# Kernel optimization log

Measured on AMD Instinct MI355X. Metric: run time of the kernel, lower is better.

Reference implementation:

```python
import jax, jax.numpy as jnp
import numpy as np

N_LAYER, N_HEAD, D_MODEL, D_K, D_HIDDEN = 8, 8, 512, 64, 2048
N_CONTEXT, N_DICT, MAG = 1024, 8192, 0.05
B, T = 8, 1024


def _sinusoidal_pos(n_context, d_model):
    i2 = np.arange(0, d_model, 2)
    inv = 1.0 / (10000.0 ** (i2 / d_model))
    ang = np.arange(n_context, dtype=np.float32)[:, None] * inv[None, :]
    pe = np.zeros((1, n_context, d_model), np.float32)
    pe[0, :, 0::2] = np.sin(ang)
    pe[0, :, 1::2] = np.cos(ang)
    return jnp.asarray(pe)


def setup_inputs() -> dict:
    key = jax.random.key(0)
    ks = jax.random.split(key, 10)
    p = lambda k, *s: jax.random.normal(k, s, jnp.float32) * MAG
    return {
        "x": jax.random.randint(ks[0], (B, T), 0, N_DICT),
        "last_only": False,
        "capture_stats": False,
        "embedding": p(ks[1], N_DICT, D_MODEL),
        "pos_embedding": _sinusoidal_pos(N_CONTEXT, D_MODEL),  # fixedpos='True', not trained
        "wq": p(ks[2], N_LAYER, N_HEAD, D_MODEL, D_K),
        "wk": p(ks[3], N_LAYER, N_HEAD, D_MODEL, D_K),
        "wv": p(ks[4], N_LAYER, N_HEAD, D_MODEL, D_MODEL),
        "mlp0": p(ks[5], N_LAYER, D_MODEL, D_HIDDEN),
        "mlpb": p(ks[6], N_LAYER, 1, D_HIDDEN),
        "mlp1": p(ks[7], N_LAYER, D_HIDDEN, D_MODEL),
        "unembedding": p(ks[8], D_MODEL, N_DICT),
        "bias": p(ks[9], 1, 1, N_DICT),
    }


def _ln(x):
    # torch LayerNorm(elementwise_affine=False, bias=False), eps=1e-5, biased var
    mu = jnp.mean(x, axis=-1, keepdims=True)
    var = jnp.mean((x - mu) ** 2, axis=-1, keepdims=True)
    return (x - mu) * jax.lax.rsqrt(var + 1e-5)


def reference(x, last_only, capture_stats, embedding, pos_embedding,
              wq, wk, wv, mlp0, mlpb, mlp1, unembedding, bias):
    del capture_stats  # stats path disabled (capture_stats=False)
    t = x.shape[1]
    h = embedding[x] + pos_embedding[:, :t, :]   # [B,T,M]
    h = _ln(h)                                    # enorm='True', lmul = 1/ldiv = 1
    mask = jnp.tril(jnp.ones((t, t), dtype=bool))

    def layer(h, params):
        wq_l, wk_l, wv_l, m0, mb, m1 = params
        q = jnp.einsum('btm,hmq->bhtq', h, wq_l)
        k = jnp.einsum('bom,hmk->bhok', h, wk_l)
        v = jnp.einsum('bom,hmv->bhov', h, wv_l)
        attn = jnp.einsum('bhtq,bhoq->bhto', q, k)
        # exp(clamp(.,max=50)) then tril then sum-normalize (NOT softmax)
        attn = jnp.where(mask, jnp.exp(jnp.minimum(attn, 50.0)), 0.0)
        attn = attn / (jnp.sum(attn, axis=-1, keepdims=True) + 1e-10)
        vsum = jnp.einsum('bhto,bhov->btv', attn, v)  # sums over heads
        h = _ln(h + vsum)                              # amul = 1, lmul = 1
        y = jax.nn.relu(jnp.einsum('btm,mh->bth', h, m0) + mb)
        y = jnp.einsum('bth,hm->btm', y, m1)
        h = _ln(h + y)                                 # pmul = 1, lmul = 1
        return h, None

    h, _ = jax.lax.scan(layer, h, (wq, wk, wv, mlp0, mlpb, mlp1))
    if last_only:
        h = h[:, -1:, :]
    return jnp.einsum('btm,md->btd', h, unembedding) + bias
```

## Files before the change

kernel.cpp:

```cpp
#include <hip/hip_runtime.h>
#include <hip/hip_bf16.h>

#define BB 8
#define TT 1024
#define DM 512
#define NH 8
#define DK 64
#define DH 2048
#define NL 8
#define ND 8192

typedef __attribute__((ext_vector_type(8))) short short8v;
typedef __attribute__((ext_vector_type(8))) _Float16 f16x8;
typedef __attribute__((ext_vector_type(4))) float f32x4;
typedef __attribute__((ext_vector_type(4))) unsigned short ushort4v;
typedef unsigned short u16;

#define MFMA16(a, b, c) __builtin_amdgcn_mfma_f32_16x16x32_bf16(a, b, c, 0, 0, 0)
#define MFMAH(a, b, c)  __builtin_amdgcn_mfma_f32_16x16x32_f16(a, b, c, 0, 0, 0)

__device__ __forceinline__ u16 bf16_bits(float f) {
  union { __hip_bfloat16 h; u16 u; } cv;
  cv.h = __float2bfloat16(f);
  return cv.u;
}
__device__ __forceinline__ float bits_to_f32(u16 u) {
  union { __hip_bfloat16 h; u16 u; } cv;
  cv.u = u;
  return __bfloat162float(cv.h);
}

__device__ __forceinline__ void gload16(const void* g, void* l) {
  __builtin_amdgcn_global_load_lds(
      (const __attribute__((address_space(1))) unsigned int*)g,
      (__attribute__((address_space(3))) unsigned int*)l, 16, 0, 0);
}

#define WAITVM(N) asm volatile("s_waitcnt vmcnt(" #N ")" ::: "memory")
#define WAITLGKM() asm volatile("s_waitcnt lgkmcnt(0)" ::: "memory")
#define BAR() { __builtin_amdgcn_s_barrier(); asm volatile("" ::: "memory"); }

#define WL_SZ 4718592
#define WR0  41943040
#define WR1 100663296

__device__ __forceinline__ void block_reduce2(float& a, float& b) {
  #pragma unroll
  for (int off = 32; off > 0; off >>= 1) {
    a += __shfl_down(a, off, 64);
    b += __shfl_down(b, off, 64);
  }
  __shared__ float sa[4], sb[4];
  int w = threadIdx.x >> 6;
  if ((threadIdx.x & 63) == 0) { sa[w] = a; sb[w] = b; }
  __syncthreads();
  if (threadIdx.x == 0) {
    sa[0] = sa[0] + sa[1] + sa[2] + sa[3];
    sb[0] = sb[0] + sb[1] + sb[2] + sb[3];
  }
  __syncthreads();
  a = sa[0]; b = sb[0];
}

__global__ __launch_bounds__(256) void embed_ln_kernel(
    const int* __restrict__ x, const float* __restrict__ emb,
    const float* __restrict__ pos, float* __restrict__ h,
    u16* __restrict__ hh, _Float16* __restrict__ hf) {
  int bt = blockIdx.x;
  int t = bt & (TT - 1);
  int tid = threadIdx.x;
  int row = x[bt];
  float v0 = emb[(size_t)row * DM + tid]       + pos[(size_t)t * DM + tid];
  float v1 = emb[(size_t)row * DM + tid + 256] + pos[(size_t)t * DM + tid + 256];
  float s = v0 + v1, sq = v0 * v0 + v1 * v1;
  block_reduce2(s, sq);
  float mu  = s * (1.0f / DM);
  float var = sq * (1.0f / DM) - mu * mu;
  float rs  = rsqrtf(var + 1e-5f);
  float r0 = (v0 - mu) * rs, r1 = (v1 - mu) * rs;
  h[(size_t)bt * DM + tid] = r0;
  h[(size_t)bt * DM + tid + 256] = r1;
  hh[(size_t)bt * DM + tid] = bf16_bits(r0);
  hh[(size_t)bt * DM + tid + 256] = bf16_bits(r1);
  hf[(size_t)bt * DM + tid] = (_Float16)r0;
  hf[(size_t)bt * DM + tid + 256] = (_Float16)r1;
}

template<bool BF16ADD>
__global__ __launch_bounds__(256) void ln_residual_kernel(
    float* __restrict__ h, const void* __restrict__ add_,
    u16* __restrict__ hh, _Float16* __restrict__ hf) {
  int bt = blockIdx.x;
  int tid = threadIdx.x;
  size_t i0 = (size_t)bt * DM + tid;
  size_t i1 = i0 + 256;
  float v0 = h[i0];
  float v1 = h[i1];
  if (BF16ADD) {
    const u16* add = (const u16*)add_;
    v0 += bits_to_f32(add[i0]);
    v1 += bits_to_f32(add[i1]);
  } else {
    const float* add = (const float*)add_;
    v0 += add[i0];
    v1 += add[i1];
  }
  float s = v0 + v1, sq = v0 * v0 + v1 * v1;
  block_reduce2(s, sq);
  float mu  = s * (1.0f / DM);
  float var = sq * (1.0f / DM) - mu * mu;
  float rs  = rsqrtf(var + 1e-5f);
  float r0 = (v0 - mu) * rs, r1 = (v1 - mu) * rs;
  h[i0] = r0;
  h[i1] = r1;
  hh[i0] = bf16_bits(r0);
  hh[i1] = bf16_bits(r1);
  hf[i0] = (_Float16)r0;
  hf[i1] = (_Float16)r1;
}

__global__ __launch_bounds__(256) void transpose_hT(
    const float* __restrict__ h, u16* __restrict__ hT) {
  __shared__ float T[64][65];
  int t0 = blockIdx.x * 64;
  int d0 = blockIdx.y * 64;
  int tid = threadIdx.x;
  #pragma unroll
  for (int rep = 0; rep < 16; ++rep) {
    int idx = rep * 256 + tid;
    int i = idx >> 6, j = idx & 63;
    T[i][j] = h[(size_t)(t0 + i) * DM + d0 + j];
  }
  __syncthreads();
  #pragma unroll
  for (int rep = 0; rep < 16; ++rep) {
    int idx = rep * 256 + tid;
    int j = idx >> 6, i = idx & 63;
    hT[(size_t)(d0 + j) * (BB * TT) + t0 + i] = bf16_bits(T[i][j]);
  }
}

__global__ __launch_bounds__(256) void prep_weights(
    const float* __restrict__ wq, const float* __restrict__ wk,
    const float* __restrict__ wv, const float* __restrict__ m0,
    const float* __restrict__ m1, const float* __restrict__ ue,
    u16* __restrict__ outus, u16* __restrict__ ueT) {
  __shared__ float T[64][65];
  int bx = blockIdx.x;
  int tid = threadIdx.x;
  if (bx >= 9216) {
    int t = bx - 9216;
    int k0 = (t & 7) * 64, n0 = (t >> 3) * 64;
    #pragma unroll
    for (int rep = 0; rep < 16; ++rep) {
      int idx = rep * 256 + tid;
      int i = idx >> 6, j = idx & 63;
      T[i][j] = ue[(size_t)(k0 + i) * ND + n0 + j];
    }
    __syncthreads();
    #pragma unroll
    for (int rep = 0; rep < 16; ++rep) {
      int idx = rep * 256 + tid;
      int j = idx >> 6, i = idx & 63;
      ueT[(size_t)(n0 + j) * DM + k0 + i] = bf16_bits(T[i][j]);
    }
    return;
  }
  int l = bx / 1152;
  int t = bx % 1152;
  u16* base = (l < 5) ? outus + WR0 + (size_t)l * WL_SZ
                      : outus + WR1 + (size_t)(l - 5) * WL_SZ;
  _Float16* qkT = (_Float16*)base;
  u16* vT2 = base + 524288;
  u16* t0o = base + 2621440;
  u16* t1o = base + 3670016;
  const float* in;
  _Float16* of = nullptr;
  u16* ob = nullptr;
  int K, Nb;
  bool vmode = false;
  if (t < 64)       { in = wq + (size_t)l * NH * DM * DK; of = qkT;          K = 512;  Nb = 64; }
  else if (t < 128) { in = wk + (size_t)l * NH * DM * DK; of = qkT + 262144; K = 512;  Nb = 64;   t -= 64; }
  else if (t < 640) { in = wv + (size_t)l * NH * DM * DM; ob = vT2;          K = 512;  Nb = 512;  t -= 128; vmode = true; }
  else if (t < 896) { in = m0 + (size_t)l * DM * DH;      ob = t0o;          K = 512;  Nb = 2048; t -= 640; }
  else              { in = m1 + (size_t)l * DH * DM;      ob = t1o;          K = 2048; Nb = 512;  t -= 896; }
  int ntx = K >> 6;
  int k0 = (t % ntx) * 64, n0 = (t / ntx) * 64;
  int g = n0 / Nb;
  const float* src = in + (size_t)g * K * Nb + (n0 - g * Nb);
  #pragma unroll
  for (int rep = 0; rep < 16; ++rep) {
    int idx = rep * 256 + tid;
    int i = idx >> 6, j = idx & 63;
    T[i][j] = src[(size_t)(k0 + i) * Nb + j];
  }
  __syncthreads();
  #pragma unroll
  for (int rep = 0; rep < 16; ++rep) {
    int idx = rep * 256 + tid;
    int j = idx >> 6, i = idx & 63;
    float v = T[i][j];
    if (vmode) {
      vT2[(size_t)(n0 - g * Nb + j) * (NH * DM) + g * Nb + k0 + i] = bf16_bits(v);
    } else if (of) {
      of[(size_t)(n0 + j) * K + k0 + i] = (_Float16)v;
    } else {
      ob[(size_t)(n0 + j) * K + k0 + i] = bf16_bits(v);
    }
  }
}

template<int MODE>
__global__ __launch_bounds__(256, 2) void gemm_mfma(
    const u16* __restrict__ A, const u16* __restrict__ Bt,
    const float* __restrict__ bias, void* __restrict__ Oo,
    int M, int N, int K) {
  __shared__ u16 As[2][8192];
  __shared__ u16 Bs[2][8192];
  int tid = threadIdx.x;
  int lane = tid & 63, w = tid >> 6;
  int l15 = lane & 15, g = lane >> 4;
  int m0 = blockIdx.x * 128, n0 = blockIdx.y * 128;
  int wr = w >> 1, wc = w & 1;
  int nt = K >> 6;

  f32x4 acc[4][4];
  #pragma unroll
  for (int i = 0; i < 4; ++i)
    #pragma unroll
    for (int j = 0; j < 4; ++j)
      #pragma unroll
      for (int r = 0; r < 4; ++r) acc[i][j][r] = 0.f;

  auto stage = [&](int t, int buf) {
    int k0 = t << 6;
    #pragma unroll
    for (int j = 0; j < 4; ++j) {
      int idx = j * 256 + tid;
      int row = idx >> 3, cs = (idx & 7) ^ (row & 7);
      gload16(A + (size_t)(m0 + row) * K + k0 + cs * 8, &As[buf][idx * 8]);
    }
    #pragma unroll
    for (int j = 0; j < 4; ++j) {
      int idx = j * 256 + tid;
      int row = idx >> 3, cs = (idx & 7) ^ (row & 7);
      gload16(Bt + (size_t)(n0 + row) * K + k0 + cs * 8, &Bs[buf][idx * 8]);
    }
  };

  stage(0, 0);
  for (int t = 0; t < nt; ++t) {
    int cur = t & 1;
    if (t + 1 < nt) {
      stage(t + 1, cur ^ 1);
      WAITVM(8);
    } else {
      WAITVM(0);
    }
    BAR();
    short8v af[4][2], bf[4][2];
    #pragma unroll
    for (int mi = 0; mi < 4; ++mi) {
      int row = wr * 64 + mi * 16 + l15;
      #pragma unroll
      for (int ks = 0; ks < 2; ++ks) {
        int ch = (ks * 4 + g) ^ (row & 7);
        af[mi][ks] = *(const short8v*)&As[cur][row * 64 + ch * 8];
      }
    }
    #pragma unroll
    for (int ni = 0; ni < 4; ++ni) {
      int row = wc * 64 + ni * 16 + l15;
      #pragma unroll
      for (int ks = 0; ks < 2; ++ks) {
        int ch = (ks * 4 + g) ^ (row & 7);
        bf[ni][ks] = *(const short8v*)&Bs[cur][row * 64 + ch * 8];
      }
    }
    __builtin_amdgcn_s_setprio(1);
    #pragma unroll
    for (int mi = 0; mi < 4; ++mi)
      #pragma unroll
      for (int ni = 0; ni < 4; ++ni) {
        acc[mi][ni] = MFMA16(af[mi][0], bf[ni][0], acc[mi][ni]);
        acc[mi][ni] = MFMA16(af[mi][1], bf[ni][1], acc[mi][ni]);
      }
    __builtin_amdgcn_s_setprio(0);
    BAR();
  }

  #pragma unroll
  for (int mi = 0; mi < 4; ++mi) {
    #pragma unroll
    for (int ni = 0; ni < 4; ++ni) {
      int mrow = m0 + wr * 64 + mi * 16 + g * 4;
      int ncol = n0 + wc * 64 + ni * 16 + l15;
      if (MODE == 1) {
        float bv = bias[ncol];
        #pragma unroll
        for (int r = 0; r < 4; ++r)
          ((u16*)Oo)[(size_t)(mrow + r) * N + ncol] =
              bf16_bits(fmaxf(acc[mi][ni][r] + bv, 0.f));
      } else {
        float bv = bias[ncol];
        #pragma unroll
        for (int r = 0; r < 4; ++r)
          ((float*)Oo)[(size_t)(mrow + r) * N + ncol] = acc[mi][ni][r] + bv;
      }
    }
  }
}

template<int MODE>
__global__ __launch_bounds__(256, 2) void gemm_n64(
    const u16* __restrict__ A, const u16* __restrict__ Bt,
    void* __restrict__ Oo, int M, int N, int K) {
  __shared__ u16 As[2][8192];
  __shared__ u16 Bs[2][4096];
  int tid = threadIdx.x;
  int lane = tid & 63, w = tid >> 6;
  int l15 = lane & 15, g = lane >> 4;
  int m0 = blockIdx.x * 128, n0 = blockIdx.y * 64;
  int wr = w >> 1, wc = w & 1;
  int nt = K >> 6;

  f32x4 acc[4][2];
  #pragma unroll
  for (int i = 0; i < 4; ++i)
    #pragma unroll
    for (int j = 0; j < 2; ++j)
      #pragma unroll
      for (int r = 0; r < 4; ++r) acc[i][j][r] = 0.f;

  auto stage = [&](int t, int buf) {
    int k0 = t << 6;
    #pragma unroll
    for (int j = 0; j < 4; ++j) {
      int idx = j * 256 + tid;
      int row = idx >> 3, cs = (idx & 7) ^ (row & 7);
      gload16(A + (size_t)(m0 + row) * K + k0 + cs * 8, &As[buf][idx * 8]);
    }
    #pragma unroll
    for (int j = 0; j < 2; ++j) {
      int idx = j * 256 + tid;
      int row = idx >> 3, cs = (idx & 7) ^ (row & 7);
      gload16(Bt + (size_t)(n0 + row) * K + k0 + cs * 8, &Bs[buf][idx * 8]);
    }
  };

  stage(0, 0);
  for (int t = 0; t < nt; ++t) {
    int cur = t & 1;
    if (t + 1 < nt) {
      stage(t + 1, cur ^ 1);
      WAITVM(6);
    } else {
      WAITVM(0);
    }
    BAR();
    short8v af[4][2], bf[2][2];
    #pragma unroll
    for (int mi = 0; mi < 4; ++mi) {
      int row = wr * 64 + mi * 16 + l15;
      #pragma unroll
      for (int ks = 0; ks < 2; ++ks) {
        int ch = (ks * 4 + g) ^ (row & 7);
        af[mi][ks] = *(const short8v*)&As[cur][row * 64 + ch * 8];
      }
    }
    #pragma unroll
    for (int ni = 0; ni < 2; ++ni) {
      int row = wc * 32 + ni * 16 + l15;
      #pragma unroll
      for (int ks = 0; ks < 2; ++ks) {
        int ch = (ks * 4 + g) ^ (row & 7);
        bf[ni][ks] = *(const short8v*)&Bs[cur][row * 64 + ch * 8];
      }
    }
    __builtin_amdgcn_s_setprio(1);
    #pragma unroll
    for (int mi = 0; mi < 4; ++mi)
      #pragma unroll
      for (int ni = 0; ni < 2; ++ni) {
        acc[mi][ni] = MFMA16(af[mi][0], bf[ni][0], acc[mi][ni]);
        acc[mi][ni] = MFMA16(af[mi][1], bf[ni][1], acc[mi][ni]);
      }
    __builtin_amdgcn_s_setprio(0);
    BAR();
  }

  #pragma unroll
  for (int mi = 0; mi < 4; ++mi) {
    #pragma unroll
    for (int ni = 0; ni < 2; ++ni) {
      int mrow = m0 + wr * 64 + mi * 16 + g * 4;
      int ncol = n0 + wc * 32 + ni * 16 + l15;
      if (MODE == 2) {
        #pragma unroll
        for (int r = 0; r < 4; ++r)
          ((float*)Oo)[(size_t)(mrow + r) * N + ncol] = acc[mi][ni][r];
      } else {
        #pragma unroll
        for (int r = 0; r < 4; ++r)
          ((u16*)Oo)[(size_t)(mrow + r) * N + ncol] = bf16_bits(acc[mi][ni][r]);
      }
    }
  }
}

__global__ __launch_bounds__(256, 2) void gemm_qk_f16(
    const _Float16* __restrict__ A, const _Float16* __restrict__ Bt,
    _Float16* __restrict__ Oq, int K) {
  __shared__ _Float16 As[2][8192];
  __shared__ _Float16 Bs[2][8192];
  int tid = threadIdx.x;
  int lane = tid & 63, w = tid >> 6;
  int l15 = lane & 15, g = lane >> 4;
  int m0 = blockIdx.x * 128, n0 = blockIdx.y * 128;
  int wr = w >> 1, wc = w & 1;
  int nt = K >> 6;

  f32x4 acc[4][4];
  #pragma unroll
  for (int i = 0; i < 4; ++i)
    #pragma unroll
    for (int j = 0; j < 4; ++j)
      #pragma unroll
      for (int r = 0; r < 4; ++r) acc[i][j][r] = 0.f;

  auto stage = [&](int t, int buf) {
    int k0 = t << 6;
    #pragma unroll
    for (int j = 0; j < 4; ++j) {
      int idx = j * 256 + tid;
      int row = idx >> 3, cs = (idx & 7) ^ (row & 7);
      gload16(A + (size_t)(m0 + row) * K + k0 + cs * 8, &As[buf][idx * 8]);
    }
    #pragma unroll
    for (int j = 0; j < 4; ++j) {
      int idx = j * 256 + tid;
      int row = idx >> 3, cs = (idx & 7) ^ (row & 7);
      gload16(Bt + (size_t)(n0 + row) * K + k0 + cs * 8, &Bs[buf][idx * 8]);
    }
  };

  stage(0, 0);
  for (int t = 0; t < nt; ++t) {
    int cur = t & 1;
    if (t + 1 < nt) {
      stage(t + 1, cur ^ 1);
      WAITVM(8);
    } else {
      WAITVM(0);
    }
    BAR();
    f16x8 af[4][2], bf[4][2];
    #pragma unroll
    for (int mi = 0; mi < 4; ++mi) {
      int row = wr * 64 + mi * 16 + l15;
      #pragma unroll
      for (int ks = 0; ks < 2; ++ks) {
        int ch = (ks * 4 + g) ^ (row & 7);
        af[mi][ks] = *(const f16x8*)&As[cur][row * 64 + ch * 8];
      }
    }
    #pragma unroll
    for (int ni = 0; ni < 4; ++ni) {
      int row = wc * 64 + ni * 16 + l15;
      #pragma unroll
      for (int ks = 0; ks < 2; ++ks) {
        int ch = (ks * 4 + g) ^ (row & 7);
        bf[ni][ks] = *(const f16x8*)&Bs[cur][row * 64 + ch * 8];
      }
    }
    __builtin_amdgcn_s_setprio(1);
    #pragma unroll
    for (int mi = 0; mi < 4; ++mi)
      #pragma unroll
      for (int ni = 0; ni < 4; ++ni) {
        acc[mi][ni] = MFMAH(af[mi][0], bf[ni][0], acc[mi][ni]);
        acc[mi][ni] = MFMAH(af[mi][1], bf[ni][1], acc[mi][ni]);
      }
    __builtin_amdgcn_s_setprio(0);
    BAR();
  }

  #pragma unroll
  for (int mi = 0; mi < 4; ++mi) {
    #pragma unroll
    for (int ni = 0; ni < 4; ++ni) {
      int mrow = m0 + wr * 64 + mi * 16 + g * 4;
      int ncol = n0 + wc * 64 + ni * 16 + l15;
      _Float16* dst = Oq;
      int nc = ncol;
      if (nc >= 512) { dst = Oq + 4194304; nc -= 512; }
      int head = nc >> 6, dk = nc & (DK - 1);
      int bb = mrow >> 10;
      #pragma unroll
      for (int r = 0; r < 4; ++r) {
        int t = (mrow + r) & (TT - 1);
        dst[(((size_t)bb * NH + head) * TT + t) * DK + dk] = (_Float16)acc[mi][ni][r];
      }
    }
  }
}

__global__ __launch_bounds__(256, 2) void attn_mfma_kernel(
    const _Float16* __restrict__ qp, const _Float16* __restrict__ kp,
    const u16* __restrict__ hT, u16* __restrict__ o) {
  __shared__ __align__(16) u16 Pl[2][64 * 64];
  __shared__ __align__(16) _Float16 Kl[2][64 * 64];
  __shared__ float rs_lds[64];

  int tid = threadIdx.x;
  int lane = tid & 63;
  int w = tid >> 6;
  int l15 = lane & 15, g = lane >> 4;
  int blk = blockIdx.x;
  int bh = blk & 63;
  int tt = 15 - (blk >> 6);
  int b = bh >> 3;

  if (tid < 64) rs_lds[tid] = 0.f;

  auto stageK = [&](int ot, int buf) {
    int ob = ot * 64;
    #pragma unroll
    for (int j = 0; j < 2; ++j) {
      int idx = j * 256 + tid;
      int row = idx >> 3, cs = (idx & 7) ^ (row & 7);
      gload16(kp + ((size_t)bh * TT + ob + row) * DK + cs * 8, &Kl[buf][idx * 8]);
    }
  };

  size_t qbase = (((size_t)bh * TT) + tt * 64 + w * 16 + l15) * DK + g * 8;
  f16x8 qf[2];
  qf[0] = *(const f16x8*)(qp + qbase);
  qf[1] = *(const f16x8*)(qp + qbase + 32);

  f32x4 oacc[4][8];
  #pragma unroll
  for (int qt = 0; qt < 4; ++qt)
    #pragma unroll
    for (int dv = 0; dv < 8; ++dv)
      #pragma unroll
      for (int r = 0; r < 4; ++r) oacc[qt][dv][r] = 0.f;

  stageK(0, 0);
  WAITVM(0);
  __syncthreads();

  for (int ot = 0; ot <= tt; ++ot) {
    int ob = ot * 64;
    bool diag = (ot == tt);
    int buf = ot & 1;
    if (ot < tt) stageK(ot + 1, buf ^ 1);
    f32x4 sacc[4];
    #pragma unroll
    for (int ct = 0; ct < 4; ++ct)
      #pragma unroll
      for (int r = 0; r < 4; ++r) sacc[ct][r] = 0.f;
    __builtin_amdgcn_s_setprio(1);
    #pragma unroll
    for (int ct = 0; ct < 4; ++ct) {
      int row = ct * 16 + l15;
      f16x8 k0 = *(const f16x8*)&Kl[buf][row * 64 + ((g) ^ (row & 7)) * 8];
      f16x8 k1 = *(const f16x8*)&Kl[buf][row * 64 + ((4 + g) ^ (row & 7)) * 8];
      sacc[ct] = MFMAH(qf[0], k0, sacc[ct]);
      sacc[ct] = MFMAH(qf[1], k1, sacc[ct]);
    }
    __builtin_amdgcn_s_setprio(0);
    size_t vbase = ((size_t)(w * 128 + l15)) * (BB * TT) + b * TT + ob + g * 8;
    short8v vf0[8];
    #pragma unroll
    for (int dv = 0; dv < 8; ++dv)
      vf0[dv] = *(const short8v*)(hT + vbase + (size_t)dv * 16 * (BB * TT));
    float psum[4] = {0.f, 0.f, 0.f, 0.f};
    #pragma unroll
    for (int ct = 0; ct < 4; ++ct) {
      #pragma unroll
      for (int r = 0; r < 4; ++r) {
        float s = sacc[ct][r];
        float p = __expf(fminf(s, 50.f));
        if (diag && (ct * 16 + l15 > w * 16 + g * 4 + r)) p = 0.f;
        psum[r] += p;
        int q = w * 16 + g * 4 + r;
        int byte = (q * 128 + (ct * 16 + l15) * 2) ^ ((q & 7) << 4);
        *(u16*)((char*)Pl[buf] + byte) = bf16_bits(p);
      }
    }
    #pragma unroll
    for (int r = 0; r < 4; ++r) {
      float v = psum[r];
      v += __shfl_xor(v, 1, 16);
      v += __shfl_xor(v, 2, 16);
      v += __shfl_xor(v, 4, 16);
      v += __shfl_xor(v, 8, 16);
      if (l15 == 0) rs_lds[w * 16 + g * 4 + r] += v;
    }
    WAITVM(8);
    WAITLGKM();
    BAR();
    short8v vf1[8];
    #pragma unroll
    for (int dv = 0; dv < 8; ++dv)
      vf1[dv] = *(const short8v*)(hT + vbase + 32 + (size_t)dv * 16 * (BB * TT));
    short8v pf[4];
    #pragma unroll
    for (int qt = 0; qt < 4; ++qt) {
      int q = qt * 16 + l15;
      int byte = (q * 128 + g * 16) ^ ((q & 7) << 4);
      pf[qt] = *(short8v*)((char*)Pl[buf] + byte);
    }
    __builtin_amdgcn_s_setprio(1);
    #pragma unroll
    for (int dv = 0; dv < 8; ++dv)
      #pragma unroll
      for (int qt = 0; qt < 4; ++qt)
        oacc[qt][dv] = MFMA16(pf[qt], vf0[dv], oacc[qt][dv]);
    __builtin_amdgcn_s_setprio(0);
    #pragma unroll
    for (int qt = 0; qt < 4; ++qt) {
      int q = qt * 16 + l15;
      int byte = (q * 128 + 64 + g * 16) ^ ((q & 7) << 4);
      pf[qt] = *(short8v*)((char*)Pl[buf] + byte);
    }
    __builtin_amdgcn_s_setprio(1);
    #pragma unroll
    for (int dv = 0; dv < 8; ++dv)
      #pragma unroll
      for (int qt = 0; qt < 4; ++qt)
        oacc[qt][dv] = MFMA16(pf[qt], vf1[dv], oacc[qt][dv]);
    __builtin_amdgcn_s_setprio(0);
  }
  __syncthreads();
  int hh2 = bh & 7;
  #pragma unroll
  for (int qt = 0; qt < 4; ++qt) {
    #pragma unroll
    for (int r = 0; r < 4; ++r) {
      int q = qt * 16 + g * 4 + r;
      float rs = 1.0f / (rs_lds[q] + 1e-10f);
      size_t rowbase = ((size_t)(b * TT + tt * 64 + q)) * (NH * DM) + hh2 * DM + w * 128 + l15;
      #pragma unroll
      for (int dv = 0; dv < 8; ++dv)
        o[rowbase + dv * 16] = bf16_bits(oacc[qt][dv][r] * rs);
    }
  }
}

extern "C" void kernel_launch(void* const* d_in, const int* in_sizes, int n_in,
                              void* d_out, int out_size, void* d_ws, size_t ws_size,
                              hipStream_t stream) {
  (void)in_sizes; (void)n_in; (void)out_size; (void)ws_size;
  const int*   x   = (const int*)d_in[0];
  const float* emb = (const float*)d_in[3];
  const float* pos = (const float*)d_in[4];
  const float* wq  = (const float*)d_in[5];
  const float* wk  = (const float*)d_in[6];
  const float* wv  = (const float*)d_in[7];
  const float* m0  = (const float*)d_in[8];
  const float* mb  = (const float*)d_in[9];
  const float* m1  = (const float*)d_in[10];
  const float* ue  = (const float*)d_in[11];
  const float* ub  = (const float*)d_in[12];
  float* out = (float*)d_out;
  float* ws  = (float*)d_ws;

  const int M = BB * TT;

  float*    h    = ws;
  u16*      hh   = (u16*)(ws + 4194304);
  _Float16* hf16 = (_Float16*)(ws + 6291456);
  float*    yb   = ws + 8388608;
  u16*      ueT  = (u16*)(ws + 12582912);

  u16* outus = (u16*)d_out;
  u16* hT   = outus;
  u16* hid  = outus + 4194304;
  u16* vsum = outus + 20971520;
  _Float16* qf16 = (_Float16*)(outus + 33554432);
  u16* Ob   = outus + 67108864;

  prep_weights<<<10240, 256, 0, stream>>>(wq, wk, wv, m0, m1, ue, outus, ueT);
  embed_ln_kernel<<<M, 256, 0, stream>>>(x, emb, pos, h, hh, hf16);
  transpose_hT<<<dim3(128, 8), 256, 0, stream>>>(h, hT);

  for (int l = 0; l < NL; ++l) {
    u16* wb = (l < 5) ? outus + WR0 + (size_t)l * WL_SZ
                      : outus + WR1 + (size_t)(l - 5) * WL_SZ;
    _Float16* wqkT = (_Float16*)wb;
    u16* wvT2 = wb + 524288;
    u16* w0T  = wb + 2621440;
    u16* w1T  = wb + 3670016;

    gemm_qk_f16<<<dim3(64, 8), 256, 0, stream>>>(hf16, wqkT, qf16, DM);
    attn_mfma_kernel<<<BB * NH * (TT / 64), 256, 0, stream>>>(
        qf16, qf16 + 4194304, hT, Ob);
    gemm_n64<4><<<dim3(64, 8), 256, 0, stream>>>(Ob, wvT2, vsum, M, DM, NH * DM);
    ln_residual_kernel<true><<<M, 256, 0, stream>>>(h, vsum, hh, hf16);
    gemm_mfma<1><<<dim3(64, 16), 256, 0, stream>>>(hh, w0T, mb + (size_t)l * DH, hid, M, DH, DM);
    gemm_n64<2><<<dim3(64, 8), 256, 0, stream>>>(hid, w1T, yb, M, DM, DH);
    ln_residual_kernel<false><<<M, 256, 0, stream>>>(h, yb, hh, hf16);
    if (l + 1 < NL)
      transpose_hT<<<dim3(128, 8), 256, 0, stream>>>(h, hT);
  }
  gemm_mfma<3><<<dim3(64, 64), 256, 0, stream>>>(hh, ueT, ub, out, M, ND, DM);
}
```

Measured before the change: 2.418 ms.

## Fuse next-layer weight transposes into attention kernel as extra blocks

Replaces the up-front transpose of all layers' weights with a transpose of layer 0 only. Each later layer's weights, and the unembedding on the last layer, are transposed by extra blocks appended to the attention kernel of the previous layer, written into a double-buffered two-layer staging area. The aim is to hide the transpose work in the tail and idle slots of the causal attention grid and to shrink the workspace footprint. The cost is a larger grid, a shared-memory union, and the attention blocks competing with the transpose blocks for bandwidth.

```diff
diff --git a/kernel.cpp b/kernel.cpp
--- a/kernel.cpp
+++ b/kernel.cpp
@@ -19,6 +19,9 @@
 #define MFMA16(a, b, c) __builtin_amdgcn_mfma_f32_16x16x32_bf16(a, b, c, 0, 0, 0)
 #define MFMAH(a, b, c)  __builtin_amdgcn_mfma_f32_16x16x32_f16(a, b, c, 0, 0, 0)
 
+#define WL_SZ 4718592
+#define WTOFF 41943040
+
 __device__ __forceinline__ u16 bf16_bits(float f) {
   union { __hip_bfloat16 h; u16 u; } cv;
   cv.h = __float2bfloat16(f);
@@ -39,10 +42,6 @@
 #define WAITVM(N) asm volatile("s_waitcnt vmcnt(" #N ")" ::: "memory")
 #define WAITLGKM() asm volatile("s_waitcnt lgkmcnt(0)" ::: "memory")
 #define BAR() { __builtin_amdgcn_s_barrier(); asm volatile("" ::: "memory"); }
-
-#define WL_SZ 4718592
-#define WR0  41943040
-#define WR1 100663296
 
 __device__ __forceinline__ void block_reduce2(float& a, float& b) {
   #pragma unroll
@@ -140,54 +139,29 @@
   }
 }
 
-__global__ __launch_bounds__(256) void prep_weights(
+__global__ __launch_bounds__(256) void transpose_layer(
     const float* __restrict__ wq, const float* __restrict__ wk,
-    const float* __restrict__ wv, const float* __restrict__ m0,
-    const float* __restrict__ m1, const float* __restrict__ ue,
-    u16* __restrict__ outus, u16* __restrict__ ueT) {
+    const float* __restrict__ wv, const float* __restrict__ w0,
+    const float* __restrict__ w1,
+    _Float16* __restrict__ qkT, u16* __restrict__ vT2,
+    u16* __restrict__ t0o, u16* __restrict__ t1o) {
   __shared__ float T[64][65];
-  int bx = blockIdx.x;
-  int tid = threadIdx.x;
-  if (bx >= 9216) {
-    int t = bx - 9216;
-    int k0 = (t & 7) * 64, n0 = (t >> 3) * 64;
-    #pragma unroll
-    for (int rep = 0; rep < 16; ++rep) {
-      int idx = rep * 256 + tid;
-      int i = idx >> 6, j = idx & 63;
-      T[i][j] = ue[(size_t)(k0 + i) * ND + n0 + j];
-    }
-    __syncthreads();
-    #pragma unroll
-    for (int rep = 0; rep < 16; ++rep) {
-      int idx = rep * 256 + tid;
-      int j = idx >> 6, i = idx & 63;
-      ueT[(size_t)(n0 + j) * DM + k0 + i] = bf16_bits(T[i][j]);
-    }
-    return;
-  }
-  int l = bx / 1152;
-  int t = bx % 1152;
-  u16* base = (l < 5) ? outus + WR0 + (size_t)l * WL_SZ
-                      : outus + WR1 + (size_t)(l - 5) * WL_SZ;
-  _Float16* qkT = (_Float16*)base;
-  u16* vT2 = base + 524288;
-  u16* t0o = base + 2621440;
-  u16* t1o = base + 3670016;
+  int t = blockIdx.x;
   const float* in;
   _Float16* of = nullptr;
   u16* ob = nullptr;
   int K, Nb;
   bool vmode = false;
-  if (t < 64)       { in = wq + (size_t)l * NH * DM * DK; of = qkT;          K = 512;  Nb = 64; }
-  else if (t < 128) { in = wk + (size_t)l * NH * DM * DK; of = qkT + 262144; K = 512;  Nb = 64;   t -= 64; }
-  else if (t < 640) { in = wv + (size_t)l * NH * DM * DM; ob = vT2;          K = 512;  Nb = 512;  t -= 128; vmode = true; }
-  else if (t < 896) { in = m0 + (size_t)l * DM * DH;      ob = t0o;          K = 512;  Nb = 2048; t -= 640; }
-  else              { in = m1 + (size_t)l * DH * DM;      ob = t1o;          K = 2048; Nb = 512;  t -= 896; }
+  if (t < 64)       { in = wq; of = qkT;          K = 512;  Nb = 64; }
+  else if (t < 128) { in = wk; of = qkT + 262144; K = 512;  Nb = 64;   t -= 64; }
+  else if (t < 640) { in = wv; ob = vT2;          K = 512;  Nb = 512;  t -= 128; vmode = true; }
+  else if (t < 896) { in = w0; ob = t0o;          K = 512;  Nb = 2048; t -= 640; }
+  else              { in = w1; ob = t1o;          K = 2048; Nb = 512;  t -= 896; }
   int ntx = K >> 6;
   int k0 = (t % ntx) * 64, n0 = (t / ntx) * 64;
   int g = n0 / Nb;
   const float* src = in + (size_t)g * K * Nb + (n0 - g * Nb);
+  int tid = threadIdx.x;
   #pragma unroll
   for (int rep = 0; rep < 16; ++rep) {
     int idx = rep * 256 + tid;
@@ -507,16 +481,80 @@
 
 __global__ __launch_bounds__(256, 2) void attn_mfma_kernel(
     const _Float16* __restrict__ qp, const _Float16* __restrict__ kp,
-    const u16* __restrict__ hT, u16* __restrict__ o) {
-  __shared__ __align__(16) u16 Pl[2][64 * 64];
-  __shared__ __align__(16) _Float16 Kl[2][64 * 64];
-  __shared__ float rs_lds[64];
-
+    const u16* __restrict__ hT, u16* __restrict__ o,
+    const float* __restrict__ gw0, const float* __restrict__ gw1,
+    const float* __restrict__ gw2, const float* __restrict__ gw3,
+    const float* __restrict__ gw4, u16* __restrict__ gdst, int gmode) {
+  __shared__ __align__(16) char smem[33024];
+
+  int blk = blockIdx.x;
   int tid = threadIdx.x;
+
+  if (blk >= 1024) {
+    float (*T)[65] = (float(*)[65])smem;
+    int t = blk - 1024;
+    if (gmode == 1) {
+      int k0 = (t & 7) * 64, n0 = (t >> 3) * 64;
+      #pragma unroll
+      for (int rep = 0; rep < 16; ++rep) {
+        int idx = rep * 256 + tid;
+        int i = idx >> 6, j = idx & 63;
+        T[i][j] = gw0[(size_t)(k0 + i) * ND + n0 + j];
+      }
+      __syncthreads();
+      #pragma unroll
+      for (int rep = 0; rep < 16; ++rep) {
+        int idx = rep * 256 + tid;
+        int j = idx >> 6, i = idx & 63;
+        gdst[(size_t)(n0 + j) * DM + k0 + i] = bf16_bits(T[i][j]);
+      }
+      return;
+    }
+    _Float16* qkT = (_Float16*)gdst;
+    u16* vT2 = gdst + 524288;
+    u16* t0o = gdst + 2621440;
+    u16* t1o = gdst + 3670016;
+    const float* in;
+    _Float16* of = nullptr;
+    u16* ob = nullptr;
+    int K, Nb;
+    bool vmode = false;
+    if (t < 64)       { in = gw0; of = qkT;          K = 512;  Nb = 64; }
+    else if (t < 128) { in = gw1; of = qkT + 262144; K = 512;  Nb = 64;   t -= 64; }
+    else if (t < 640) { in = gw2; ob = vT2;          K = 512;  Nb = 512;  t -= 128; vmode = true; }
+    else if (t < 896) { in = gw3; ob = t0o;          K = 512;  Nb = 2048; t -= 640; }
+    else              { in = gw4; ob = t1o;          K = 2048; Nb = 512;  t -= 896; }
+    int ntx = K >> 6;
+    int k0 = (t % ntx) * 64, n0 = (t / ntx) * 64;
+    int g2 = n0 / Nb;
+    const float* src = in + (size_t)g2 * K * Nb + (n0 - g2 * Nb);
+    #pragma unroll
+    for (int rep = 0; rep < 16; ++rep) {
+      int idx = rep * 256 + tid;
+      int i = idx >> 6, j = idx & 63;
+      T[i][j] = src[(size_t)(k0 + i) * Nb + j];
+    }
+    __syncthreads();
+    #pragma unroll
+    for (int rep = 0; rep < 16; ++rep) {
+      int idx = rep * 256 + tid;
+      int j = idx >> 6, i = idx & 63;
+      float v = T[i][j];
+      if (vmode) {
+        vT2[(size_t)(n0 - g2 * Nb + j) * (NH * DM) + g2 * Nb + k0 + i] = bf16_bits(v);
+      } else if (of) {
+        of[(size_t)(n0 + j) * K + k0 + i] = (_Float16)v;
+      } else {
+        ob[(size_t)(n0 + j) * K + k0 + i] = bf16_bits(v);
+      }
+    }
+    return;
+  }
+
+  float* rs_lds = (float*)(smem + 32768);
   int lane = tid & 63;
   int w = tid >> 6;
   int l15 = lane & 15, g = lane >> 4;
-  int blk = blockIdx.x;
   int bh = blk & 63;
   int tt = 15 - (blk >> 6);
   int b = bh >> 3;
@@ -524,12 +562,13 @@
   if (tid < 64) rs_lds[tid] = 0.f;
 
   auto stageK = [&](int ot, int buf) {
-    int ob = ot * 64;
+    int ob2 = ot * 64;
     #pragma unroll
     for (int j = 0; j < 2; ++j) {
       int idx = j * 256 + tid;
       int row = idx >> 3, cs = (idx & 7) ^ (row & 7);
-      gload16(kp + ((size_t)bh * TT + ob + row) * DK + cs * 8, &Kl[buf][idx * 8]);
+      gload16(kp + ((size_t)bh * TT + ob2 + row) * DK + cs * 8,
+              smem + 16384 + buf * 8192 + idx * 16);
     }
   };
 
@@ -551,10 +590,11 @@
   __syncthreads();
 
   for (int ot = 0; ot <= tt; ++ot) {
-    int ob = ot * 64;
+    int ob2 = ot * 64;
     bool diag = (ot == tt);
     int buf = ot & 1;
     if (ot < tt) stageK(ot + 1, buf ^ 1);
+    const _Float16* KlB = (const _Float16*)(smem + 16384 + buf * 8192);
     f32x4 sacc[4];
     #pragma unroll
     for (int ct = 0; ct < 4; ++ct)
@@ -564,13 +604,13 @@
     #pragma unroll
     for (int ct = 0; ct < 4; ++ct) {
       int row = ct * 16 + l15;
-      f16x8 k0 = *(const f16x8*)&Kl[buf][row * 64 + ((g) ^ (row & 7)) * 8];
-      f16x8 k1 = *(const f16x8*)&Kl[buf][row * 64 + ((4 + g) ^ (row & 7)) * 8];
-      sacc[ct] = MFMAH(qf[0], k0, sacc[ct]);
-      sacc[ct] = MFMAH(qf[1], k1, sacc[ct]);
+      f16x8 k0v = *(const f16x8*)&KlB[row * 64 + ((g) ^ (row & 7)) * 8];
+      f16x8 k1v = *(const f16x8*)&KlB[row * 64 + ((4 + g) ^ (row & 7)) * 8];
+      sacc[ct] = MFMAH(qf[0], k0v, sacc[ct]);
+      sacc[ct] = MFMAH(qf[1], k1v, sacc[ct]);
     }
     __builtin_amdgcn_s_setprio(0);
-    size_t vbase = ((size_t)(w * 128 + l15)) * (BB * TT) + b * TT + ob + g * 8;
+    size_t vbase = ((size_t)(w * 128 + l15)) * (BB * TT) + b * TT + ob2 + g * 8;
     short8v vf0[8];
     #pragma unroll
     for (int dv = 0; dv < 8; ++dv)
@@ -586,7 +626,7 @@
         psum[r] += p;
         int q = w * 16 + g * 4 + r;
         int byte = (q * 128 + (ct * 16 + l15) * 2) ^ ((q & 7) << 4);
-        *(u16*)((char*)Pl[buf] + byte) = bf16_bits(p);
+        *(u16*)(smem + buf * 8192 + byte) = bf16_bits(p);
       }
     }
     #pragma unroll
@@ -610,7 +650,7 @@
     for (int qt = 0; qt < 4; ++qt) {
       int q = qt * 16 + l15;
       int byte = (q * 128 + g * 16) ^ ((q & 7) << 4);
-      pf[qt] = *(short8v*)((char*)Pl[buf] + byte);
+      pf[qt] = *(short8v*)(smem + buf * 8192 + byte);
     }
     __builtin_amdgcn_s_setprio(1);
     #pragma unroll
@@ -623,7 +663,7 @@
     for (int qt = 0; qt < 4; ++qt) {
       int q = qt * 16 + l15;
       int byte = (q * 128 + 64 + g * 16) ^ ((q & 7) << 4);
-      pf[qt] = *(short8v*)((char*)Pl[buf] + byte);
+      pf[qt] = *(short8v*)(smem + buf * 8192 + byte);
     }
     __builtin_amdgcn_s_setprio(1);
     #pragma unroll
@@ -680,23 +720,34 @@
   u16* hid  = outus + 4194304;
   u16* vsum = outus + 20971520;
   _Float16* qf16 = (_Float16*)(outus + 33554432);
+  u16* wT   = outus + WTOFF;
   u16* Ob   = outus + 67108864;
 
-  prep_weights<<<10240, 256, 0, stream>>>(wq, wk, wv, m0, m1, ue, outus, ueT);
+  transpose_layer<<<1152, 256, 0, stream>>>(
+      wq, wk, wv, m0, m1,
+      (_Float16*)wT, wT + 524288, wT + 2621440, wT + 3670016);
   embed_ln_kernel<<<M, 256, 0, stream>>>(x, emb, pos, h, hh, hf16);
   transpose_hT<<<dim3(128, 8), 256, 0, stream>>>(h, hT);
 
   for (int l = 0; l < NL; ++l) {
-    u16* wb = (l < 5) ? outus + WR0 + (size_t)l * WL_SZ
-                      : outus + WR1 + (size_t)(l - 5) * WL_SZ;
+    u16* wb = wT + (size_t)(l & 1) * WL_SZ;
+    u16* wn = wT + (size_t)((l + 1) & 1) * WL_SZ;
     _Float16* wqkT = (_Float16*)wb;
     u16* wvT2 = wb + 524288;
     u16* w0T  = wb + 2621440;
     u16* w1T  = wb + 3670016;
 
     gemm_qk_f16<<<dim3(64, 8), 256, 0, stream>>>(hf16, wqkT, qf16, DM);
-    attn_mfma_kernel<<<BB * NH * (TT / 64), 256, 0, stream>>>(
-        qf16, qf16 + 4194304, hT, Ob);
+    if (l + 1 < NL) {
+      attn_mfma_kernel<<<1024 + 1152, 256, 0, stream>>>(
+          qf16, qf16 + 4194304, hT, Ob,
+          wq + (size_t)(l + 1) * NH * DM * DK, wk + (size_t)(l + 1) * NH * DM * DK,
+          wv + (size_t)(l + 1) * NH * DM * DM, m0 + (size_t)(l + 1) * DM * DH,
+          m1 + (size_t)(l + 1) * DH * DM, wn, 0);
+    } else {
+      attn_mfma_kernel<<<1024 + 1024, 256, 0, stream>>>(
+          qf16, qf16 + 4194304, hT, Ob, ue, ue, ue, ue, ue, ueT, 1);
+    }
     gemm_n64<4><<<dim3(64, 8), 256, 0, stream>>>(Ob, wvT2, vsum, M, DM, NH * DM);
     ln_residual_kernel<true><<<M, 256, 0, stream>>>(h, vsum, hh, hf16);
     gemm_mfma<1><<<dim3(64, 16), 256, 0, stream>>>(hh, w0T, mb + (size_t)l * DH, hid, M, DH, DM);
```

Measured after the change: 2.229 ms. 7.8% less time.
